# Kernel optimization log

Hardware: AMD Instinct MI355X
Metric: run time of the kernel (lower is better)

The kernel has to match this reference:

```python
import jax, jax.numpy as jnp
import numpy as np


def _generate_linear_ibf(intervals, coeffs):
    # Faithful vectorization of generate_linear_ibf:
    # block i (i < n_vars): ones(n_vars,2); row i <- intervals[i]; row 0 *= coeffs[i]
    # block n_vars:         ones(n_vars,2); row 0 *= coeffs[n_vars]
    n_vars = intervals.shape[0]
    blocks = jnp.ones((n_vars + 1, n_vars, 2), dtype=coeffs.dtype)
    idx = jnp.arange(n_vars)
    blocks = blocks.at[idx, idx, :].set(intervals)            # set interval rows first
    blocks = blocks.at[:, 0, :].multiply(coeffs[:, None])     # then scale row 0 (matches torch order)
    return blocks.reshape((n_vars + 1) * n_vars, 2)


def setup_inputs() -> dict:
    key = jax.random.key(0)
    ks = jax.random.split(key, 6)
    n_vars, K = 4096, 4096
    return {
        "layer_inputs_under": jax.random.normal(ks[0], (K, n_vars + 1), dtype=jnp.float32),
        "layer_inputs_over": jax.random.normal(ks[1], (K, n_vars + 1), dtype=jnp.float32),
        "layer_inputs_under_degrees": jnp.ones((n_vars,), dtype=jnp.float32),
        "layer_inputs_over_degrees": jnp.ones((n_vars,), dtype=jnp.float32),
        "intervals": jax.random.uniform(ks[2], (n_vars, 2), dtype=jnp.float32),
        "node_pos_weights": jax.random.uniform(ks[3], (K,), dtype=jnp.float32),
        "node_neg_weights": -jax.random.uniform(ks[4], (K,), dtype=jnp.float32),
        "node_bias": jax.random.normal(ks[5], (1,), dtype=jnp.float32),
    }


def reference(layer_inputs_under, layer_inputs_over,
              layer_inputs_under_degrees, layer_inputs_over_degrees,
              intervals, node_pos_weights, node_neg_weights, node_bias):
    n_vars = intervals.shape[0]
    # ibf_tensor_prod_input_weights (generic nonzero path): (1,K) @ (K, n_vars+1)
    # NOTE: in torch, input_under[-1] += bias on a (1, n_vars+1) tensor adds the bias
    # to the entire (single) row; we reproduce that exactly.
    under_coeffs = (node_neg_weights @ layer_inputs_over
                    + node_pos_weights @ layer_inputs_under) + node_bias  # (n_vars+1,)
    over_coeffs = (node_pos_weights @ layer_inputs_over
                   + node_neg_weights @ layer_inputs_under) + node_bias   # (n_vars+1,)

    # degrees from both products are ones(n_vars); elementwise max is ones
    under_degree = jnp.ones((n_vars,), dtype=under_coeffs.dtype)
    over_degree = jnp.ones((n_vars,), dtype=over_coeffs.dtype)

    input_under = _generate_linear_ibf(intervals, under_coeffs)  # ((n_vars+1)*n_vars, 2)
    input_over = _generate_linear_ibf(intervals, over_coeffs)

    # activation == 'linear' branch
    return (input_under, input_over, under_degree, over_degree)
```

## Files before the change

kernel.cpp:

```cpp
#include <hip/hip_runtime.h>

__global__ __launch_bounds__(256) void gemv4(
    const float* __restrict__ U, const float* __restrict__ O,
    const float* __restrict__ pos, const float* __restrict__ neg,
    float* __restrict__ su, float* __restrict__ so,
    int K, int ncols, int rows_per_chunk) {
  int j = blockIdx.x * blockDim.x + threadIdx.x;
  int k0 = blockIdx.y * rows_per_chunk;
  int k1 = k0 + rows_per_chunk;
  if (k1 > K) k1 = K;
  if (j >= ncols) return;

  float acc_u = 0.f, acc_o = 0.f;
  const float* Up = U + (size_t)k0 * ncols + j;
  const float* Op = O + (size_t)k0 * ncols + j;
  for (int k = k0; k < k1; ++k) {
    float p = pos[k];
    float n = neg[k];
    float a = *Up; Up += ncols;
    float b = *Op; Op += ncols;
    acc_u = fmaf(p, a, acc_u);
    acc_u = fmaf(n, b, acc_u);
    acc_o = fmaf(p, b, acc_o);
    acc_o = fmaf(n, a, acc_o);
  }
  atomicAdd(&su[j], acc_u);
  atomicAdd(&so[j], acc_o);
}

__global__ __launch_bounds__(256) void fill4(
    const float* __restrict__ intervals,
    const float* __restrict__ su, const float* __restrict__ so,
    const float* __restrict__ bias_p,
    float* __restrict__ outU, float* __restrict__ outO,
    float* __restrict__ degs,
    int n_vars, int shift, int mask, int n4total) {
  int i4 = blockIdx.x * blockDim.x + threadIdx.x;

  if (i4 < 2 * n_vars) degs[i4] = 1.0f;
  if (i4 >= n4total) return;

  int i = i4 << 2;
  int blk = i >> shift;
  int within = i & mask;
  int r0 = within >> 1;

  float4 base = make_float4(1.f, 1.f, 1.f, 1.f);
  if (r0 == blk) {
    base.x = intervals[2 * blk];
    base.y = intervals[2 * blk + 1];
  } else if (r0 + 1 == blk) {
    base.z = intervals[2 * blk];
    base.w = intervals[2 * blk + 1];
  }

  float4 vu = base, vo = base;
  if (r0 == 0) {
    float b = bias_p[0];
    float cu = su[blk] + b;
    float co = so[blk] + b;
    vu.x = base.x * cu; vu.y = base.y * cu;
    vo.x = base.x * co; vo.y = base.y * co;
  }

  reinterpret_cast<float4*>(outU)[i4] = vu;
  reinterpret_cast<float4*>(outO)[i4] = vo;
}

__global__ __launch_bounds__(256) void fill_scalar(
    const float* __restrict__ intervals,
    const float* __restrict__ su, const float* __restrict__ so,
    const float* __restrict__ bias_p,
    float* __restrict__ outU, float* __restrict__ outO,
    float* __restrict__ degs,
    int n_vars, long long S) {
  long long tid = (long long)blockIdx.x * blockDim.x + threadIdx.x;
  long long nthreads = (long long)gridDim.x * blockDim.x;
  if (tid < 2 * n_vars) degs[tid] = 1.0f;
  int two_n = 2 * n_vars;
  for (long long i = tid; i < S; i += nthreads) {
    int blk = (int)(i / two_n);
    int within = (int)(i - (long long)blk * two_n);
    int r = within >> 1;
    int c = within & 1;
    float v = 1.f;
    if (r == blk) v = intervals[2 * r + c];
    float vu = v, vo = v;
    if (r == 0) {
      float b = bias_p[0];
      vu = v * (su[blk] + b);
      vo = v * (so[blk] + b);
    }
    outU[i] = vu;
    outO[i] = vo;
  }
}

extern "C" void kernel_launch(void* const* d_in, const int* in_sizes, int n_in,
                              void* d_out, int out_size, void* d_ws, size_t ws_size,
                              hipStream_t stream) {
  const float* U         = (const float*)d_in[0];
  const float* O         = (const float*)d_in[1];
  const float* intervals = (const float*)d_in[4];
  const float* pos       = (const float*)d_in[5];
  const float* neg       = (const float*)d_in[6];
  const float* bias      = (const float*)d_in[7];

  const int n_vars = in_sizes[4] / 2;
  const int K      = in_sizes[5];
  const int ncols  = n_vars + 1;

  float* su = (float*)d_ws;
  float* so = su + ncols;
  hipMemsetAsync(d_ws, 0, (size_t)2 * ncols * sizeof(float), stream);

  const int rows_per_chunk = 64;
  dim3 ggrid((ncols + 255) / 256, (K + rows_per_chunk - 1) / rows_per_chunk);
  gemv4<<<ggrid, 256, 0, stream>>>(U, O, pos, neg, su, so, K, ncols, rows_per_chunk);

  const long long S = (long long)ncols * n_vars * 2;
  float* outU = (float*)d_out;
  float* outO = outU + S;
  float* degs = outU + 2 * S;

  const int two_n = 2 * n_vars;
  const bool pow2 = two_n > 0 && (two_n & (two_n - 1)) == 0 && (two_n % 4 == 0);
  if (pow2 && S / 4 < (1LL << 31)) {
    int shift = __builtin_ctz((unsigned)two_n);
    int n4 = (int)(S / 4);
    long long nthreads = n4 > 2 * n_vars ? n4 : 2 * n_vars;
    int blocks = (int)((nthreads + 255) / 256);
    fill4<<<blocks, 256, 0, stream>>>(intervals, su, so, bias, outU, outO, degs,
                                      n_vars, shift, two_n - 1, n4);
  } else {
    int blocks = 4096;
    fill_scalar<<<blocks, 256, 0, stream>>>(intervals, su, so, bias, outU, outO, degs,
                                            n_vars, S);
  }
}
```

Before: 385.3 us.

## Fuse GEMV and output fill into one grid, replace atomics with partial-sum finish kernel

The GEMV and the bulk output fill now run as one launch: the first blocks compute column partial sums over K-chunks, and the remaining blocks write the constant and interval pattern. This lets the large output write overlap with the input reads. Per-chunk partials go to workspace instead of atomics, which removes the memset. A small finish kernel reduces the partials, adds the bias and writes the row-0 coefficients and degrees. The GEMV inner loop is also unrolled by 4, and there are fewer, larger K-chunks. That gives less GEMV block parallelism and adds an extra launch with strided scattered writes.

```diff
diff --git a/kernel.cpp b/kernel.cpp
--- a/kernel.cpp
+++ b/kernel.cpp
@@ -1,82 +1,83 @@
 #include <hip/hip_runtime.h>
 
-__global__ __launch_bounds__(256) void gemv4(
+#define TPB 256
+
+__global__ __launch_bounds__(TPB) void fused_gemv_fill(
     const float* __restrict__ U, const float* __restrict__ O,
     const float* __restrict__ pos, const float* __restrict__ neg,
-    float* __restrict__ su, float* __restrict__ so,
-    int K, int ncols, int rows_per_chunk) {
-  int j = blockIdx.x * blockDim.x + threadIdx.x;
-  int k0 = blockIdx.y * rows_per_chunk;
-  int k1 = k0 + rows_per_chunk;
-  if (k1 > K) k1 = K;
-  if (j >= ncols) return;
+    const float* __restrict__ intervals,
+    float* __restrict__ pu, float* __restrict__ po,
+    float* __restrict__ outU, float* __restrict__ outO,
+    int K, int ncols,
+    int col_tiles, int rpc,
+    int shift, int mask, int n4total, int n_gemv_blocks) {
+  int b = blockIdx.x;
 
-  float acc_u = 0.f, acc_o = 0.f;
-  const float* Up = U + (size_t)k0 * ncols + j;
-  const float* Op = O + (size_t)k0 * ncols + j;
-  for (int k = k0; k < k1; ++k) {
-    float p = pos[k];
-    float n = neg[k];
-    float a = *Up; Up += ncols;
-    float b = *Op; Op += ncols;
-    acc_u = fmaf(p, a, acc_u);
-    acc_u = fmaf(n, b, acc_u);
-    acc_o = fmaf(p, b, acc_o);
-    acc_o = fmaf(n, a, acc_o);
+  if (b < n_gemv_blocks) {
+    int tile  = b % col_tiles;
+    int chunk = b / col_tiles;
+    int j = tile * TPB + threadIdx.x;
+    if (j >= ncols) return;
+    int k0 = chunk * rpc;
+    int k1 = k0 + rpc; if (k1 > K) k1 = K;
+
+    const float* Uq = U + (size_t)k0 * ncols + j;
+    const float* Oq = O + (size_t)k0 * ncols + j;
+    const size_t st = (size_t)ncols;
+    float au = 0.f, ao = 0.f;
+    int k = k0;
+    for (; k + 4 <= k1; k += 4) {
+      float p0 = pos[k],   p1 = pos[k+1], p2 = pos[k+2], p3 = pos[k+3];
+      float n0 = neg[k],   n1 = neg[k+1], n2 = neg[k+2], n3 = neg[k+3];
+      float a0 = Uq[0], a1 = Uq[st], a2 = Uq[2*st], a3 = Uq[3*st];
+      float b0 = Oq[0], b1 = Oq[st], b2 = Oq[2*st], b3 = Oq[3*st];
+      Uq += 4*st; Oq += 4*st;
+      au = fmaf(p0, a0, au); au = fmaf(n0, b0, au);
+      ao = fmaf(p0, b0, ao); ao = fmaf(n0, a0, ao);
+      au = fmaf(p1, a1, au); au = fmaf(n1, b1, au);
+      ao = fmaf(p1, b1, ao); ao = fmaf(n1, a1, ao);
+      au = fmaf(p2, a2, au); au = fmaf(n2, b2, au);
+      ao = fmaf(p2, b2, ao); ao = fmaf(n2, a2, ao);
+      au = fmaf(p3, a3, au); au = fmaf(n3, b3, au);
+      ao = fmaf(p3, b3, ao); ao = fmaf(n3, a3, ao);
+    }
+    for (; k < k1; ++k) {
+      float p = pos[k], n = neg[k];
+      float a = Uq[0], bb = Oq[0];
+      Uq += st; Oq += st;
+      au = fmaf(p, a, au); au = fmaf(n, bb, au);
+      ao = fmaf(p, bb, ao); ao = fmaf(n, a, ao);
+    }
+    pu[(size_t)chunk * ncols + j] = au;
+    po[(size_t)chunk * ncols + j] = ao;
+    return;
   }
-  atomicAdd(&su[j], acc_u);
-  atomicAdd(&so[j], acc_o);
-}
 
-__global__ __launch_bounds__(256) void fill4(
-    const float* __restrict__ intervals,
-    const float* __restrict__ su, const float* __restrict__ so,
-    const float* __restrict__ bias_p,
-    float* __restrict__ outU, float* __restrict__ outO,
-    float* __restrict__ degs,
-    int n_vars, int shift, int mask, int n4total) {
-  int i4 = blockIdx.x * blockDim.x + threadIdx.x;
-
-  if (i4 < 2 * n_vars) degs[i4] = 1.0f;
+  int i4 = (b - n_gemv_blocks) * TPB + threadIdx.x;
   if (i4 >= n4total) return;
-
   int i = i4 << 2;
   int blk = i >> shift;
   int within = i & mask;
   int r0 = within >> 1;
 
-  float4 base = make_float4(1.f, 1.f, 1.f, 1.f);
+  float4 v = make_float4(1.f, 1.f, 1.f, 1.f);
   if (r0 == blk) {
-    base.x = intervals[2 * blk];
-    base.y = intervals[2 * blk + 1];
+    v.x = intervals[2 * blk];
+    v.y = intervals[2 * blk + 1];
   } else if (r0 + 1 == blk) {
-    base.z = intervals[2 * blk];
-    base.w = intervals[2 * blk + 1];
+    v.z = intervals[2 * blk];
+    v.w = intervals[2 * blk + 1];
   }
-
-  float4 vu = base, vo = base;
-  if (r0 == 0) {
-    float b = bias_p[0];
-    float cu = su[blk] + b;
-    float co = so[blk] + b;
-    vu.x = base.x * cu; vu.y = base.y * cu;
-    vo.x = base.x * co; vo.y = base.y * co;
-  }
-
-  reinterpret_cast<float4*>(outU)[i4] = vu;
-  reinterpret_cast<float4*>(outO)[i4] = vo;
+  reinterpret_cast<float4*>(outU)[i4] = v;
+  reinterpret_cast<float4*>(outO)[i4] = v;
 }
 
-__global__ __launch_bounds__(256) void fill_scalar(
+__global__ __launch_bounds__(TPB) void fill_scalar(
     const float* __restrict__ intervals,
-    const float* __restrict__ su, const float* __restrict__ so,
-    const float* __restrict__ bias_p,
     float* __restrict__ outU, float* __restrict__ outO,
-    float* __restrict__ degs,
     int n_vars, long long S) {
   long long tid = (long long)blockIdx.x * blockDim.x + threadIdx.x;
   long long nthreads = (long long)gridDim.x * blockDim.x;
-  if (tid < 2 * n_vars) degs[tid] = 1.0f;
   int two_n = 2 * n_vars;
   for (long long i = tid; i < S; i += nthreads) {
     int blk = (int)(i / two_n);
@@ -85,14 +86,36 @@
     int c = within & 1;
     float v = 1.f;
     if (r == blk) v = intervals[2 * r + c];
-    float vu = v, vo = v;
-    if (r == 0) {
-      float b = bias_p[0];
-      vu = v * (su[blk] + b);
-      vo = v * (so[blk] + b);
-    }
-    outU[i] = vu;
-    outO[i] = vo;
+    outU[i] = v;
+    outO[i] = v;
+  }
+}
+
+__global__ __launch_bounds__(TPB) void finish(
+    const float* __restrict__ pu, const float* __restrict__ po,
+    const float* __restrict__ intervals, const float* __restrict__ bias_p,
+    float* __restrict__ outU, float* __restrict__ outO,
+    float* __restrict__ degs,
+    int ncols, int n_vars, int nchunks) {
+  int t = blockIdx.x * TPB + threadIdx.x;
+  int two_n = 2 * n_vars;
+  if (t < two_n) degs[t] = 1.0f;
+
+  if (t < ncols) {
+    float s = bias_p[0];
+    for (int c = 0; c < nchunks; ++c) s += pu[(size_t)c * ncols + t];
+    float vx = s, vy = s;
+    if (t == 0) { vx = intervals[0] * s; vy = intervals[1] * s; }
+    size_t off = (size_t)t * two_n;
+    outU[off] = vx; outU[off + 1] = vy;
+  } else if (t < 2 * ncols) {
+    int j = t - ncols;
+    float s = bias_p[0];
+    for (int c = 0; c < nchunks; ++c) s += po[(size_t)c * ncols + j];
+    float vx = s, vy = s;
+    if (j == 0) { vx = intervals[0] * s; vy = intervals[1] * s; }
+    size_t off = (size_t)j * two_n;
+    outO[off] = vx; outO[off + 1] = vy;
   }
 }
 
@@ -110,13 +133,15 @@
   const int K      = in_sizes[5];
   const int ncols  = n_vars + 1;
 
-  float* su = (float*)d_ws;
-  float* so = su + ncols;
-  hipMemsetAsync(d_ws, 0, (size_t)2 * ncols * sizeof(float), stream);
+  int nchunks = 32;
+  while (nchunks > 1 && (size_t)2 * nchunks * ncols * sizeof(float) > ws_size)
+    nchunks >>= 1;
+  float* pu = (float*)d_ws;
+  float* po = pu + (size_t)nchunks * ncols;
 
-  const int rows_per_chunk = 64;
-  dim3 ggrid((ncols + 255) / 256, (K + rows_per_chunk - 1) / rows_per_chunk);
-  gemv4<<<ggrid, 256, 0, stream>>>(U, O, pos, neg, su, so, K, ncols, rows_per_chunk);
+  const int col_tiles = (ncols + TPB - 1) / TPB;
+  const int rpc = (K + nchunks - 1) / nchunks;
+  const int n_gemv_blocks = col_tiles * nchunks;
 
   const long long S = (long long)ncols * n_vars * 2;
   float* outU = (float*)d_out;
@@ -124,17 +149,24 @@
   float* degs = outU + 2 * S;
 
   const int two_n = 2 * n_vars;
-  const bool pow2 = two_n > 0 && (two_n & (two_n - 1)) == 0 && (two_n % 4 == 0);
+  const bool pow2 = two_n > 0 && (two_n & (two_n - 1)) == 0;
+
   if (pow2 && S / 4 < (1LL << 31)) {
     int shift = __builtin_ctz((unsigned)two_n);
     int n4 = (int)(S / 4);
-    long long nthreads = n4 > 2 * n_vars ? n4 : 2 * n_vars;
-    int blocks = (int)((nthreads + 255) / 256);
-    fill4<<<blocks, 256, 0, stream>>>(intervals, su, so, bias, outU, outO, degs,
-                                      n_vars, shift, two_n - 1, n4);
+    int fill_blocks = (n4 + TPB - 1) / TPB;
+    int grid = n_gemv_blocks + fill_blocks;
+    fused_gemv_fill<<<grid, TPB, 0, stream>>>(
+        U, O, pos, neg, intervals, pu, po, outU, outO,
+        K, ncols, col_tiles, rpc, shift, two_n - 1, n4, n_gemv_blocks);
   } else {
-    int blocks = 4096;
-    fill_scalar<<<blocks, 256, 0, stream>>>(intervals, su, so, bias, outU, outO, degs,
-                                            n_vars, S);
+    fused_gemv_fill<<<n_gemv_blocks, TPB, 0, stream>>>(
+        U, O, pos, neg, intervals, pu, po, outU, outO,
+        K, ncols, col_tiles, rpc, 0, 0, 0, n_gemv_blocks);
+    fill_scalar<<<4096, TPB, 0, stream>>>(intervals, outU, outO, n_vars, S);
   }
+
+  int nB = (2 * ncols > two_n ? 2 * ncols : two_n);
+  finish<<<(nB + TPB - 1) / TPB, TPB, 0, stream>>>(
+      pu, po, intervals, bias, outU, outO, degs, ncols, n_vars, nchunks);
 }
```

Measured after the change: 386.4 us. No clear change (+0.3%).
